# Optimization experiments

Hardware: AMD Instinct MI355X
Metric: run time of the kernel (lower is better)

## Reference

```python
import jax, jax.numpy as jnp
import numpy as np

WIDTH = 300  # CFG.width
H = 128


def _lstm_layer(x, W_ih, W_hh, b_ih, b_hh):
    # x: [B, T, D]; W_ih: [4H, D]; W_hh: [4H, H]; biases: [4H]
    B = x.shape[0]
    # precompute input contributions for all timesteps: [T, B, 4H]
    xg = jnp.einsum('btd,gd->tbg', x, W_ih) + (b_ih + b_hh)

    def step(carry, xg_t):
        h, c = carry
        g = xg_t + h @ W_hh.T  # [B, 4H]
        i, f, gg, o = jnp.split(g, 4, axis=-1)  # PyTorch gate order i,f,g,o
        i = jax.nn.sigmoid(i)
        f = jax.nn.sigmoid(f)
        gg = jnp.tanh(gg)
        o = jax.nn.sigmoid(o)
        c = f * c + i * gg
        h = o * jnp.tanh(c)
        return (h, c), h

    h0 = jnp.zeros((B, H), x.dtype)
    c0 = jnp.zeros((B, H), x.dtype)
    _, hs = jax.lax.scan(step, (h0, c0), xg)  # hs: [T, B, H]
    return jnp.transpose(hs, (1, 0, 2))  # [B, T, H]


def setup_inputs() -> dict:
    key = jax.random.key(0)
    ks = jax.random.split(key, 16)
    s = 0.05
    B, D, T = 512, 80, WIDTH
    return {
        'x': jax.random.normal(ks[0], (B, D, T), jnp.float32),
        'W_ih0': jax.random.normal(ks[1], (4 * H, D), jnp.float32) * s,
        'W_hh0': jax.random.normal(ks[2], (4 * H, H), jnp.float32) * s,
        'b_ih0': jax.random.normal(ks[3], (4 * H,), jnp.float32) * s,
        'b_hh0': jax.random.normal(ks[4], (4 * H,), jnp.float32) * s,
        'W_ih1': jax.random.normal(ks[5], (4 * H, H), jnp.float32) * s,
        'W_hh1': jax.random.normal(ks[6], (4 * H, H), jnp.float32) * s,
        'b_ih1': jax.random.normal(ks[7], (4 * H,), jnp.float32) * s,
        'b_hh1': jax.random.normal(ks[8], (4 * H,), jnp.float32) * s,
        'fc1_w': jax.random.normal(ks[9], (64, H), jnp.float32) * s,
        'fc1_b': jax.random.normal(ks[10], (64,), jnp.float32) * s,
        'fc2_w': jax.random.normal(ks[11], (32, 64), jnp.float32) * s,
        'fc2_b': jax.random.normal(ks[12], (32,), jnp.float32) * s,
        'fc3_w': jax.random.normal(ks[13], (2, 32), jnp.float32) * s,
        'fc3_b': jax.random.normal(ks[14], (2,), jnp.float32) * s,
    }


def reference(x, W_ih0, W_hh0, b_ih0, b_hh0, W_ih1, W_hh1, b_ih1, b_hh1,
              fc1_w, fc1_b, fc2_w, fc2_b, fc3_w, fc3_b):
    # input.transpose(-1,-2): [B, D, T] -> [B, T, D]
    seq = jnp.transpose(x, (0, 2, 1))
    h1 = _lstm_layer(seq, W_ih0, W_hh0, b_ih0, b_hh0)
    h2 = _lstm_layer(h1, W_ih1, W_hh1, b_ih1, b_hh1)
    out = h2[:, WIDTH - 1, :]  # [B, H]
    # _fc head (dropout is identity in eval mode)
    out = jax.nn.relu(out @ fc1_w.T + fc1_b)
    out = jax.nn.relu(out @ fc2_w.T + fc2_b)
    out = out @ fc3_w.T + fc3_b
    return out
```

## Files before the change

### kernel.cpp

```cpp
#include <hip/hip_runtime.h>


typedef _Float16 f16;
typedef _Float16 f16x8 __attribute__((ext_vector_type(8)));
typedef float f32x4 __attribute__((ext_vector_type(4)));
typedef unsigned u32x2 __attribute__((ext_vector_type(2)));

#define T_SEQ 300
#define D_IN  80
#define HDIM  128
#define B_ALL 512
#define B_TILE 16
#define N_PROD 32
#define N_WG_TOT 64

#define XT_BYTES  ((size_t)B_ALL * T_SEQ * D_IN * 2)
#define H1_BYTES  ((size_t)T_SEQ * B_ALL * HDIM * 2)
#define FLAGS_OFF (XT_BYTES + H1_BYTES)
#define FLAGS_BYTES ((size_t)N_PROD * T_SEQ * 4)
#define HSTEP_BYTES ((uint64_t)B_ALL * HDIM * 2)

__device__ __forceinline__ float sigm(float x) {
    return __builtin_amdgcn_rcpf(1.0f + __builtin_amdgcn_exp2f(-1.44269504f * x));
}
__device__ __forceinline__ float tanh_fast(float x) {
    return 1.0f - 2.0f * __builtin_amdgcn_rcpf(1.0f + __builtin_amdgcn_exp2f(2.88539008f * x));
}

__device__ __forceinline__ void wg_barrier_lds() {
    asm volatile("s_waitcnt lgkmcnt(0)" ::: "memory");
    __builtin_amdgcn_sched_barrier(0);
    __builtin_amdgcn_s_barrier();
    __builtin_amdgcn_sched_barrier(0);
}
__device__ __forceinline__ void vm_drain() {
    asm volatile("s_waitcnt vmcnt(0)" ::: "memory");
    __builtin_amdgcn_sched_barrier(0);
}

__global__ __launch_bounds__(256) void k_prep(const float* __restrict__ x,
                                              f16* __restrict__ xT) {
    __shared__ f16 tile[D_IN][T_SEQ + 8];
    const int b = blockIdx.x;
    const int tid = threadIdx.x;
    const float* xb = x + (size_t)b * D_IN * T_SEQ;
    for (int i = tid; i < D_IN * T_SEQ; i += 256) {
        int d = i / T_SEQ;
        int t = i - d * T_SEQ;
        tile[d][t] = (f16)xb[i];
    }
    __syncthreads();
    f16* outb = xT + (size_t)b * T_SEQ * D_IN;
    for (int i = tid; i < T_SEQ * (D_IN / 8); i += 256) {
        int t  = i / (D_IN / 8);
        int dc = i - t * (D_IN / 8);
        f16x8 v;
#pragma unroll
        for (int e = 0; e < 8; ++e) v[e] = tile[dc * 8 + e][t];
        *(f16x8*)(outb + t * D_IN + dc * 8) = v;
    }
}

__device__ __forceinline__ f16x8 load_wfrag(const float* __restrict__ W,
                                            int row, int ld, int k0, int kmax) {
    f16x8 v;
#pragma unroll
    for (int e = 0; e < 8; ++e) {
        int k = k0 + e;
        v[e] = (k < kmax) ? (f16)W[row * ld + k] : (f16)0.0f;
    }
    return v;
}

__global__ __launch_bounds__(512, 2) void k_lstm(
    const f16* __restrict__ xT, f16* __restrict__ h1ws, int* __restrict__ flags,
    const float* __restrict__ Wih0, const float* __restrict__ Whh0,
    const float* __restrict__ bih0, const float* __restrict__ bhh0,
    const float* __restrict__ Wih1, const float* __restrict__ Whh1,
    const float* __restrict__ bih1, const float* __restrict__ bhh1,
    const float* __restrict__ fc1w, const float* __restrict__ fc1b,
    const float* __restrict__ fc2w, const float* __restrict__ fc2b,
    const float* __restrict__ fc3w, const float* __restrict__ fc3b,
    float* __restrict__ out)
{
    const int tid = threadIdx.x;
    const int wv  = tid >> 6;
    const int l   = tid & 63;
    const int l16 = l & 15;
    const int lg  = l >> 4;
    const int wg  = blockIdx.x;
    const int u   = wv * 16 + l16;

    __shared__ __align__(16) f16 hbuf[2][16 * HDIM];
    __shared__ float h2buf[16][HDIM];
    __shared__ float a1buf[16][64];
    __shared__ float a2buf[16][33];

    for (int i = tid; i < 16 * HDIM; i += 512) hbuf[0][i] = (f16)0.0f;

    float cst[4] = {0.f, 0.f, 0.f, 0.f};

    if (wg < N_PROD) {
        const int wgb = wg;
        f16x8 wih[4][3], whh[4][4];
        float biasv[4];
#pragma unroll
        for (int nt = 0; nt < 4; ++nt) {
            int gate = nt * 128 + u;
            biasv[nt] = bih0[gate] + bhh0[gate];
#pragma unroll
            for (int kc = 0; kc < 4; ++kc)
                whh[nt][kc] = load_wfrag(Whh0, gate, HDIM, kc * 32 + lg * 8, HDIM);
#pragma unroll
            for (int kc = 0; kc < 3; ++kc)
                wih[nt][kc] = load_wfrag(Wih0, gate, D_IN, kc * 32 + lg * 8, D_IN);
        }

        const f16* xrowp = xT + (size_t)(wgb * B_TILE + l16) * T_SEQ * D_IN + lg * 8;
        const uint64_t xrowu = (uint64_t)(uintptr_t)xrowp;
        const uint64_t flagu = (uint64_t)(uintptr_t)(flags + wgb * T_SEQ);
        const int sbr = tid >> 5;
        const int sob = (tid & 31) * 8;
        const int sswz = (((sob >> 4) ^ (sbr & 7)) << 4) + (sob & 8);
        const uint64_t sdst0 = (uint64_t)(uintptr_t)h1ws +
                               (uint64_t)(wgb * B_TILE + sbr) * 256 + sob;

        f16x8 p0 = *(const f16x8*)(xrowp);
        f16x8 p1 = *(const f16x8*)(xrowp + 32);
        f16x8 p2 = *(const f16x8*)(xrowp + 64);
        f16x8 xA0 = *(const f16x8*)(xrowp + D_IN);
        f16x8 xA1 = *(const f16x8*)(xrowp + D_IN + 32);
        f16x8 xA2 = *(const f16x8*)(xrowp + D_IN + 64);
        f32x4 acc_x[4];
#pragma unroll
        for (int nt = 0; nt < 4; ++nt) {
            f32x4 a = {biasv[nt], biasv[nt], biasv[nt], biasv[nt]};
            a = __builtin_amdgcn_mfma_f32_16x16x32_f16(p0, wih[nt][0], a, 0, 0, 0);
            a = __builtin_amdgcn_mfma_f32_16x16x32_f16(p1, wih[nt][1], a, 0, 0, 0);
            a = __builtin_amdgcn_mfma_f32_16x16x32_f16(p2, wih[nt][2], a, 0, 0, 0);
            acc_x[nt] = a;
        }
        __syncthreads();

        auto pstep = [&](int t, f16x8& xc0, f16x8& xc1, f16x8& xc2,
                         f16x8& xn0, f16x8& xn1, f16x8& xn2) {
            const f16* cur = hbuf[t & 1];
            f16* nxt = hbuf[(t + 1) & 1];
            f16x8 ha[4];
#pragma unroll
            for (int kc = 0; kc < 4; ++kc) {
                int chunk = kc * 4 + lg;
                ha[kc] = *(const f16x8*)(cur + l16 * HDIM + ((chunk ^ (l16 & 7)) << 3));
            }
            if (t >= 1) {
                u32x2 hval = *(const u32x2*)((const char*)cur + sbr * 256 + sswz);
                uint64_t dst = sdst0 + (uint64_t)(t - 1) * HSTEP_BYTES;
                asm volatile("global_store_dwordx2 %0, %1, off sc0 sc1"
                             :: "v"(dst), "v"(hval) : "memory");
            }
            {
                int tl = (t + 2 < T_SEQ) ? t + 2 : T_SEQ - 1;
                uint64_t xa = xrowu + (uint64_t)tl * (D_IN * 2);
                asm volatile("global_load_dwordx4 %0, %1, off"            : "=v"(xn0) : "v"(xa) : "memory");
                asm volatile("global_load_dwordx4 %0, %1, off offset:64"  : "=v"(xn1) : "v"(xa) : "memory");
                asm volatile("global_load_dwordx4 %0, %1, off offset:128" : "=v"(xn2) : "v"(xa) : "memory");
            }
            f32x4 acc[4];
#pragma unroll
            for (int nt = 0; nt < 4; ++nt) {
                f32x4 a = acc_x[nt];
                a = __builtin_amdgcn_mfma_f32_16x16x32_f16(ha[0], whh[nt][0], a, 0, 0, 0);
                a = __builtin_amdgcn_mfma_f32_16x16x32_f16(ha[1], whh[nt][1], a, 0, 0, 0);
                a = __builtin_amdgcn_mfma_f32_16x16x32_f16(ha[2], whh[nt][2], a, 0, 0, 0);
                a = __builtin_amdgcn_mfma_f32_16x16x32_f16(ha[3], whh[nt][3], a, 0, 0, 0);
                acc[nt] = a;
            }
            asm volatile("s_waitcnt vmcnt(4)" ::: "memory");
            __builtin_amdgcn_sched_barrier(0);
#pragma unroll
            for (int nt = 0; nt < 4; ++nt) {
                f32x4 a = {biasv[nt], biasv[nt], biasv[nt], biasv[nt]};
                a = __builtin_amdgcn_mfma_f32_16x16x32_f16(xc0, wih[nt][0], a, 0, 0, 0);
                a = __builtin_amdgcn_mfma_f32_16x16x32_f16(xc1, wih[nt][1], a, 0, 0, 0);
                a = __builtin_amdgcn_mfma_f32_16x16x32_f16(xc2, wih[nt][2], a, 0, 0, 0);
                acc_x[nt] = a;
            }
#pragma unroll
            for (int r = 0; r < 4; ++r) {
                float iv = sigm(acc[0][r]);
                float fv = sigm(acc[1][r]);
                float gv = tanh_fast(acc[2][r]);
                float ov = sigm(acc[3][r]);
                float cn = fv * cst[r] + iv * gv;
                cst[r] = cn;
                f16 hh = (f16)(ov * tanh_fast(cn));
                int br = lg * 4 + r;
                nxt[br * HDIM + ((((unsigned)u >> 3) ^ (br & 7)) << 3) + (u & 7)] = hh;
            }
            asm volatile("s_waitcnt vmcnt(3)" ::: "memory");
            __builtin_amdgcn_sched_barrier(0);
            wg_barrier_lds();
            if (tid == 0 && t >= 1) {
                unsigned one = 1;
                uint64_t fa = flagu + (uint64_t)(t - 1) * 4;
                asm volatile("global_store_dword %0, %1, off sc0 sc1"
                             :: "v"(fa), "v"(one) : "memory");
            }
        };

        f16x8 xB0, xB1, xB2;
        for (int t = 0; t < T_SEQ; t += 2) {
            pstep(t,     xA0, xA1, xA2, xB0, xB1, xB2);
            pstep(t + 1, xB0, xB1, xB2, xA0, xA1, xA2);
        }
        {
            const f16* cur = hbuf[T_SEQ & 1];
            u32x2 hval = *(const u32x2*)((const char*)cur + sbr * 256 + sswz);
            uint64_t dst = sdst0 + (uint64_t)(T_SEQ - 1) * HSTEP_BYTES;
            asm volatile("global_store_dwordx2 %0, %1, off sc0 sc1"
                         :: "v"(dst), "v"(hval) : "memory");
            vm_drain();
            wg_barrier_lds();
            if (tid == 0) {
                unsigned one = 1;
                uint64_t fa = flagu + (uint64_t)(T_SEQ - 1) * 4;
                asm volatile("global_store_dword %0, %1, off sc0 sc1"
                             :: "v"(fa), "v"(one) : "memory");
            }
        }
        return;
    }

    {
        const int wgb = wg - N_PROD;
        f16x8 wih[4][4], whh[4][4];
        float biasv[4];
#pragma unroll
        for (int nt = 0; nt < 4; ++nt) {
            int gate = nt * 128 + u;
            biasv[nt] = bih1[gate] + bhh1[gate];
#pragma unroll
            for (int kc = 0; kc < 4; ++kc) {
                wih[nt][kc] = load_wfrag(Wih1, gate, HDIM, kc * 32 + lg * 8, HDIM);
                whh[nt][kc] = load_wfrag(Whh1, gate, HDIM, kc * 32 + lg * 8, HDIM);
            }
        }
        __syncthreads();

        const uint64_t flagu = (uint64_t)(uintptr_t)(flags + wgb * T_SEQ);
        const uint64_t xbase = (uint64_t)(uintptr_t)h1ws +
                               (uint64_t)(wgb * B_TILE + l16) * 256 + (uint64_t)lg * 16;

        unsigned pv = 0;
#pragma unroll 1
        for (int s = 0; s < 2; ++s) {
            uint64_t fa = flagu + (uint64_t)s * 4;
            do {
                asm volatile("global_load_dword %0, %1, off sc0 sc1"
                             : "=v"(pv) : "v"(fa) : "memory");
                asm volatile("s_waitcnt vmcnt(0)" ::: "memory");
            } while (pv == 0);
        }
        f16x8 q0, q1, q2, q3, xA0, xA1, xA2, xA3;
        {
            uint64_t a0 = xbase;
            asm volatile("global_load_dwordx4 %0, %1, off sc0 sc1"            : "=v"(q0) : "v"(a0) : "memory");
            asm volatile("global_load_dwordx4 %0, %1, off offset:64 sc0 sc1"  : "=v"(q1) : "v"(a0) : "memory");
            asm volatile("global_load_dwordx4 %0, %1, off offset:128 sc0 sc1" : "=v"(q2) : "v"(a0) : "memory");
            asm volatile("global_load_dwordx4 %0, %1, off offset:192 sc0 sc1" : "=v"(q3) : "v"(a0) : "memory");
            uint64_t a1 = xbase + HSTEP_BYTES;
            asm volatile("global_load_dwordx4 %0, %1, off sc0 sc1"            : "=v"(xA0) : "v"(a1) : "memory");
            asm volatile("global_load_dwordx4 %0, %1, off offset:64 sc0 sc1"  : "=v"(xA1) : "v"(a1) : "memory");
            asm volatile("global_load_dwordx4 %0, %1, off offset:128 sc0 sc1" : "=v"(xA2) : "v"(a1) : "memory");
            asm volatile("global_load_dwordx4 %0, %1, off offset:192 sc0 sc1" : "=v"(xA3) : "v"(a1) : "memory");
            vm_drain();
        }
        f32x4 acc_x[4];
#pragma unroll
        for (int nt = 0; nt < 4; ++nt) {
            f32x4 a = {biasv[nt], biasv[nt], biasv[nt], biasv[nt]};
            a = __builtin_amdgcn_mfma_f32_16x16x32_f16(q0, wih[nt][0], a, 0, 0, 0);
            a = __builtin_amdgcn_mfma_f32_16x16x32_f16(q1, wih[nt][1], a, 0, 0, 0);
            a = __builtin_amdgcn_mfma_f32_16x16x32_f16(q2, wih[nt][2], a, 0, 0, 0);
            a = __builtin_amdgcn_mfma_f32_16x16x32_f16(q3, wih[nt][3], a, 0, 0, 0);
            acc_x[nt] = a;
        }
        {
            uint64_t pf = flagu + 2 * 4;
            asm volatile("global_load_dword %0, %1, off sc0 sc1"
                         : "=v"(pv) : "v"(pf) : "memory");
        }

        float hlast[4] = {0.f, 0.f, 0.f, 0.f};

        auto cstep = [&](int t, f16x8& c0, f16x8& c1, f16x8& c2, f16x8& c3,
                         f16x8& n0, f16x8& n1, f16x8& n2, f16x8& n3) {
            const f16* cur = hbuf[t & 1];
            f16* nxt = hbuf[(t + 1) & 1];
            vm_drain();
            if (t + 2 < T_SEQ) {
                if (pv == 0) {
                    uint64_t fa = flagu + (uint64_t)(t + 2) * 4;
                    do {
                        asm volatile("global_load_dword %0, %1, off sc0 sc1"
                                     : "=v"(pv) : "v"(fa) : "memory");
                        asm volatile("s_waitcnt vmcnt(0)" ::: "memory");
                    } while (pv == 0);
                }
                uint64_t na = xbase + (uint64_t)(t + 2) * HSTEP_BYTES;
                asm volatile("global_load_dwordx4 %0, %1, off sc0 sc1"            : "=v"(n0) : "v"(na) : "memory");
                asm volatile("global_load_dwordx4 %0, %1, off offset:64 sc0 sc1"  : "=v"(n1) : "v"(na) : "memory");
                asm volatile("global_load_dwordx4 %0, %1, off offset:128 sc0 sc1" : "=v"(n2) : "v"(na) : "memory");
                asm volatile("global_load_dwordx4 %0, %1, off offset:192 sc0 sc1" : "=v"(n3) : "v"(na) : "memory");
                if (t + 3 < T_SEQ) {
                    uint64_t pf = flagu + (uint64_t)(t + 3) * 4;
                    asm volatile("global_load_dword %0, %1, off sc0 sc1"
                                 : "=v"(pv) : "v"(pf) : "memory");
                }
            }
            f16x8 ha[4];
#pragma unroll
            for (int kc = 0; kc < 4; ++kc) {
                int chunk = kc * 4 + lg;
                ha[kc] = *(const f16x8*)(cur + l16 * HDIM + ((chunk ^ (l16 & 7)) << 3));
            }
            f32x4 acc[4];
#pragma unroll
            for (int nt = 0; nt < 4; ++nt) {
                f32x4 a = acc_x[nt];
                a = __builtin_amdgcn_mfma_f32_16x16x32_f16(ha[0], whh[nt][0], a, 0, 0, 0);
                a = __builtin_amdgcn_mfma_f32_16x16x32_f16(ha[1], whh[nt][1], a, 0, 0, 0);
                a = __builtin_amdgcn_mfma_f32_16x16x32_f16(ha[2], whh[nt][2], a, 0, 0, 0);
                a = __builtin_amdgcn_mfma_f32_16x16x32_f16(ha[3], whh[nt][3], a, 0, 0, 0);
                acc[nt] = a;
            }
            if (t + 1 < T_SEQ) {
#pragma unroll
                for (int nt = 0; nt < 4; ++nt) {
                    f32x4 a = {biasv[nt], biasv[nt], biasv[nt], biasv[nt]};
                    a = __builtin_amdgcn_mfma_f32_16x16x32_f16(c0, wih[nt][0], a, 0, 0, 0);
                    a = __builtin_amdgcn_mfma_f32_16x16x32_f16(c1, wih[nt][1], a, 0, 0, 0);
                    a = __builtin_amdgcn_mfma_f32_16x16x32_f16(c2, wih[nt][2], a, 0, 0, 0);
                    a = __builtin_amdgcn_mfma_f32_16x16x32_f16(c3, wih[nt][3], a, 0, 0, 0);
                    acc_x[nt] = a;
                }
            }
#pragma unroll
            for (int r = 0; r < 4; ++r) {
                float iv = sigm(acc[0][r]);
                float fv = sigm(acc[1][r]);
                float gv = tanh_fast(acc[2][r]);
                float ov = sigm(acc[3][r]);
                float cn = fv * cst[r] + iv * gv;
                cst[r] = cn;
                float hv = ov * tanh_fast(cn);
                hlast[r] = hv;
                int br = lg * 4 + r;
                nxt[br * HDIM + ((((unsigned)u >> 3) ^ (br & 7)) << 3) + (u & 7)] = (f16)hv;
            }
            wg_barrier_lds();
        };

        f16x8 xB0, xB1, xB2, xB3;
        for (int t = 0; t < T_SEQ; t += 2) {
            cstep(t,     xA0, xA1, xA2, xA3, xB0, xB1, xB2, xB3);
            cstep(t + 1, xB0, xB1, xB2, xB3, xA0, xA1, xA2, xA3);
        }

#pragma unroll
        for (int r = 0; r < 4; ++r) h2buf[lg * 4 + r][u] = hlast[r];
        __syncthreads();

        for (int i = tid; i < 16 * 64; i += 512) {
            int b = i >> 6, o = i & 63;
            float s = fc1b[o];
            for (int k = 0; k < HDIM; ++k) s += h2buf[b][k] * fc1w[o * HDIM + k];
            a1buf[b][o] = fmaxf(s, 0.f);
        }
        __syncthreads();
        if (tid < 16 * 32) {
            int b = tid >> 5, o = tid & 31;
            float s = fc2b[o];
            for (int k = 0; k < 64; ++k) s += a1buf[b][k] * fc2w[o * 64 + k];
            a2buf[b][o] = fmaxf(s, 0.f);
        }
        __syncthreads();
        if (tid < 32) {
            int b = tid >> 1, o = tid & 1;
            float s = fc3b[o];
            for (int k = 0; k < 32; ++k) s += a2buf[b][k] * fc3w[o * 32 + k];
            out[(wgb * B_TILE + b) * 2 + o] = s;
        }
    }
}

extern "C" void kernel_launch(void* const* d_in, const int* in_sizes, int n_in,
                              void* d_out, int out_size, void* d_ws, size_t ws_size,
                              hipStream_t stream)
{
    const float* x    = (const float*)d_in[0];
    const float* Wih0 = (const float*)d_in[1];
    const float* Whh0 = (const float*)d_in[2];
    const float* bih0 = (const float*)d_in[3];
    const float* bhh0 = (const float*)d_in[4];
    const float* Wih1 = (const float*)d_in[5];
    const float* Whh1 = (const float*)d_in[6];
    const float* bih1 = (const float*)d_in[7];
    const float* bhh1 = (const float*)d_in[8];
    const float* fc1w = (const float*)d_in[9];
    const float* fc1b = (const float*)d_in[10];
    const float* fc2w = (const float*)d_in[11];
    const float* fc2b = (const float*)d_in[12];
    const float* fc3w = (const float*)d_in[13];
    const float* fc3b = (const float*)d_in[14];

    f16* xT    = (f16*)d_ws;
    f16* h1    = (f16*)((char*)d_ws + XT_BYTES);
    int* flags = (int*)((char*)d_ws + FLAGS_OFF);

    hipMemsetAsync(flags, 0, FLAGS_BYTES, stream);
    k_prep<<<B_ALL, 256, 0, stream>>>(x, xT);
    k_lstm<<<N_WG_TOT, 512, 0, stream>>>(xT, h1, flags, Wih0, Whh0, bih0, bhh0,
                                         Wih1, Whh1, bih1, bhh1,
                                         fc1w, fc1b, fc2w, fc2b, fc3w, fc3b,
                                         (float*)d_out);
}
```

Measured before the change: 383.0 us.

## Fuse LSTM gate math, double-buffer input projections, store h directly from registers

Replaces separate sigmoid/tanh calls with a fused gate routine that shares reciprocals, cutting transcendental and rcp ops per cell. Producer and consumer loops now ping-pong two input-projection accumulators and issue the next step's x-projection MFMAs before the recurrent MFMAs, taking them off the serial dependency chain. The producer writes h directly from registers with short stores each step, so it no longer reads back LDS to store the previous step's h. The tradeoffs are more accumulator registers, finer-grained global stores, and changed vmcnt waits that must still order the h stores before each flag is published.

```diff
diff --git a/kernel.cpp b/kernel.cpp
--- a/kernel.cpp
+++ b/kernel.cpp
@@ -4,7 +4,6 @@
 typedef _Float16 f16;
 typedef _Float16 f16x8 __attribute__((ext_vector_type(8)));
 typedef float f32x4 __attribute__((ext_vector_type(4)));
-typedef unsigned u32x2 __attribute__((ext_vector_type(2)));
 
 #define T_SEQ 300
 #define D_IN  80
@@ -20,13 +19,6 @@
 #define FLAGS_BYTES ((size_t)N_PROD * T_SEQ * 4)
 #define HSTEP_BYTES ((uint64_t)B_ALL * HDIM * 2)
 
-__device__ __forceinline__ float sigm(float x) {
-    return __builtin_amdgcn_rcpf(1.0f + __builtin_amdgcn_exp2f(-1.44269504f * x));
-}
-__device__ __forceinline__ float tanh_fast(float x) {
-    return 1.0f - 2.0f * __builtin_amdgcn_rcpf(1.0f + __builtin_amdgcn_exp2f(2.88539008f * x));
-}
-
 __device__ __forceinline__ void wg_barrier_lds() {
     asm volatile("s_waitcnt lgkmcnt(0)" ::: "memory");
     __builtin_amdgcn_sched_barrier(0);
@@ -36,6 +28,23 @@
 __device__ __forceinline__ void vm_drain() {
     asm volatile("s_waitcnt vmcnt(0)" ::: "memory");
     __builtin_amdgcn_sched_barrier(0);
+}
+__device__ __forceinline__ void vm_wait7() {
+    asm volatile("s_waitcnt vmcnt(7)" ::: "memory");
+    __builtin_amdgcn_sched_barrier(0);
+}
+
+__device__ __forceinline__ float lstm_fuse(float ai, float af, float ag, float ao,
+                                           float& c) {
+    float Ei = __builtin_amdgcn_exp2f(-1.44269504f * ai);
+    float Ef = __builtin_amdgcn_exp2f(-1.44269504f * af);
+    float Eo = __builtin_amdgcn_exp2f(-1.44269504f * ao);
+    float Eg = __builtin_amdgcn_exp2f( 2.88539008f * ag);
+    float ig = (Eg - 1.0f) * __builtin_amdgcn_rcpf((1.0f + Ei) * (Eg + 1.0f));
+    float fs = __builtin_amdgcn_rcpf(1.0f + Ef);
+    c = fs * c + ig;
+    float Ec = __builtin_amdgcn_exp2f(2.88539008f * c);
+    return (Ec - 1.0f) * __builtin_amdgcn_rcpf((1.0f + Eo) * (Ec + 1.0f));
 }
 
 __global__ __launch_bounds__(256) void k_prep(const float* __restrict__ x,
@@ -116,34 +125,37 @@
                 wih[nt][kc] = load_wfrag(Wih0, gate, D_IN, kc * 32 + lg * 8, D_IN);
         }
 
-        const f16* xrowp = xT + (size_t)(wgb * B_TILE + l16) * T_SEQ * D_IN + lg * 8;
-        const uint64_t xrowu = (uint64_t)(uintptr_t)xrowp;
+        const uint64_t xrowu = (uint64_t)(uintptr_t)(
+            xT + (size_t)(wgb * B_TILE + l16) * T_SEQ * D_IN + lg * 8);
         const uint64_t flagu = (uint64_t)(uintptr_t)(flags + wgb * T_SEQ);
-        const int sbr = tid >> 5;
-        const int sob = (tid & 31) * 8;
-        const int sswz = (((sob >> 4) ^ (sbr & 7)) << 4) + (sob & 8);
-        const uint64_t sdst0 = (uint64_t)(uintptr_t)h1ws +
-                               (uint64_t)(wgb * B_TILE + sbr) * 256 + sob;
-
-        f16x8 p0 = *(const f16x8*)(xrowp);
-        f16x8 p1 = *(const f16x8*)(xrowp + 32);
-        f16x8 p2 = *(const f16x8*)(xrowp + 64);
-        f16x8 xA0 = *(const f16x8*)(xrowp + D_IN);
-        f16x8 xA1 = *(const f16x8*)(xrowp + D_IN + 32);
-        f16x8 xA2 = *(const f16x8*)(xrowp + D_IN + 64);
-        f32x4 acc_x[4];
+        uint64_t haddr = (uint64_t)(uintptr_t)h1ws +
+                         (uint64_t)(wgb * B_TILE + lg * 4) * 256 + (uint64_t)u * 2;
+
+        f16x8 p0, p1, p2, xA0, xA1, xA2, xB0, xB1, xB2;
+        asm volatile("global_load_dwordx4 %0, %1, off"            : "=v"(p0)  : "v"(xrowu) : "memory");
+        asm volatile("global_load_dwordx4 %0, %1, off offset:64"  : "=v"(p1)  : "v"(xrowu) : "memory");
+        asm volatile("global_load_dwordx4 %0, %1, off offset:128" : "=v"(p2)  : "v"(xrowu) : "memory");
+        {
+            uint64_t xa = xrowu + (uint64_t)(D_IN * 2);
+            asm volatile("global_load_dwordx4 %0, %1, off"            : "=v"(xA0) : "v"(xa) : "memory");
+            asm volatile("global_load_dwordx4 %0, %1, off offset:64"  : "=v"(xA1) : "v"(xa) : "memory");
+            asm volatile("global_load_dwordx4 %0, %1, off offset:128" : "=v"(xA2) : "v"(xa) : "memory");
+        }
+        vm_drain();
+        f32x4 accA[4], accB[4];
 #pragma unroll
         for (int nt = 0; nt < 4; ++nt) {
             f32x4 a = {biasv[nt], biasv[nt], biasv[nt], biasv[nt]};
             a = __builtin_amdgcn_mfma_f32_16x16x32_f16(p0, wih[nt][0], a, 0, 0, 0);
             a = __builtin_amdgcn_mfma_f32_16x16x32_f16(p1, wih[nt][1], a, 0, 0, 0);
             a = __builtin_amdgcn_mfma_f32_16x16x32_f16(p2, wih[nt][2], a, 0, 0, 0);
-            acc_x[nt] = a;
+            accA[nt] = a;
         }
         __syncthreads();
 
         auto pstep = [&](int t, f16x8& xc0, f16x8& xc1, f16x8& xc2,
-                         f16x8& xn0, f16x8& xn1, f16x8& xn2) {
+                         f16x8& xn0, f16x8& xn1, f16x8& xn2,
+                         f32x4 (&accX)[4], f32x4 (&accN)[4]) {
             const f16* cur = hbuf[t & 1];
             f16* nxt = hbuf[(t + 1) & 1];
             f16x8 ha[4];
@@ -151,12 +163,6 @@
             for (int kc = 0; kc < 4; ++kc) {
                 int chunk = kc * 4 + lg;
                 ha[kc] = *(const f16x8*)(cur + l16 * HDIM + ((chunk ^ (l16 & 7)) << 3));
-            }
-            if (t >= 1) {
-                u32x2 hval = *(const u32x2*)((const char*)cur + sbr * 256 + sswz);
-                uint64_t dst = sdst0 + (uint64_t)(t - 1) * HSTEP_BYTES;
-                asm volatile("global_store_dwordx2 %0, %1, off sc0 sc1"
-                             :: "v"(dst), "v"(hval) : "memory");
             }
             {
                 int tl = (t + 2 < T_SEQ) ? t + 2 : T_SEQ - 1;
@@ -165,40 +171,40 @@
                 asm volatile("global_load_dwordx4 %0, %1, off offset:64"  : "=v"(xn1) : "v"(xa) : "memory");
                 asm volatile("global_load_dwordx4 %0, %1, off offset:128" : "=v"(xn2) : "v"(xa) : "memory");
             }
+            vm_wait7();
+#pragma unroll
+            for (int nt = 0; nt < 4; ++nt) {
+                f32x4 a = {biasv[nt], biasv[nt], biasv[nt], biasv[nt]};
+                a = __builtin_amdgcn_mfma_f32_16x16x32_f16(xc0, wih[nt][0], a, 0, 0, 0);
+                a = __builtin_amdgcn_mfma_f32_16x16x32_f16(xc1, wih[nt][1], a, 0, 0, 0);
+                a = __builtin_amdgcn_mfma_f32_16x16x32_f16(xc2, wih[nt][2], a, 0, 0, 0);
+                accN[nt] = a;
+            }
             f32x4 acc[4];
 #pragma unroll
             for (int nt = 0; nt < 4; ++nt) {
-                f32x4 a = acc_x[nt];
+                f32x4 a = accX[nt];
                 a = __builtin_amdgcn_mfma_f32_16x16x32_f16(ha[0], whh[nt][0], a, 0, 0, 0);
                 a = __builtin_amdgcn_mfma_f32_16x16x32_f16(ha[1], whh[nt][1], a, 0, 0, 0);
                 a = __builtin_amdgcn_mfma_f32_16x16x32_f16(ha[2], whh[nt][2], a, 0, 0, 0);
                 a = __builtin_amdgcn_mfma_f32_16x16x32_f16(ha[3], whh[nt][3], a, 0, 0, 0);
                 acc[nt] = a;
             }
-            asm volatile("s_waitcnt vmcnt(4)" ::: "memory");
-            __builtin_amdgcn_sched_barrier(0);
-#pragma unroll
-            for (int nt = 0; nt < 4; ++nt) {
-                f32x4 a = {biasv[nt], biasv[nt], biasv[nt], biasv[nt]};
-                a = __builtin_amdgcn_mfma_f32_16x16x32_f16(xc0, wih[nt][0], a, 0, 0, 0);
-                a = __builtin_amdgcn_mfma_f32_16x16x32_f16(xc1, wih[nt][1], a, 0, 0, 0);
-                a = __builtin_amdgcn_mfma_f32_16x16x32_f16(xc2, wih[nt][2], a, 0, 0, 0);
-                acc_x[nt] = a;
-            }
+            unsigned hb[4];
 #pragma unroll
             for (int r = 0; r < 4; ++r) {
-                float iv = sigm(acc[0][r]);
-                float fv = sigm(acc[1][r]);
-                float gv = tanh_fast(acc[2][r]);
-                float ov = sigm(acc[3][r]);
-                float cn = fv * cst[r] + iv * gv;
-                cst[r] = cn;
-                f16 hh = (f16)(ov * tanh_fast(cn));
+                float hv = lstm_fuse(acc[0][r], acc[1][r], acc[2][r], acc[3][r], cst[r]);
+                f16 hh = (f16)hv;
+                hb[r] = (unsigned)__builtin_bit_cast(unsigned short, hh);
                 int br = lg * 4 + r;
                 nxt[br * HDIM + ((((unsigned)u >> 3) ^ (br & 7)) << 3) + (u & 7)] = hh;
             }
-            asm volatile("s_waitcnt vmcnt(3)" ::: "memory");
-            __builtin_amdgcn_sched_barrier(0);
+            asm volatile("global_store_short %0, %1, off sc0 sc1"            :: "v"(haddr), "v"(hb[0]) : "memory");
+            asm volatile("global_store_short %0, %1, off offset:256 sc0 sc1" :: "v"(haddr), "v"(hb[1]) : "memory");
+            asm volatile("global_store_short %0, %1, off offset:512 sc0 sc1" :: "v"(haddr), "v"(hb[2]) : "memory");
+            asm volatile("global_store_short %0, %1, off offset:768 sc0 sc1" :: "v"(haddr), "v"(hb[3]) : "memory");
+            haddr += HSTEP_BYTES;
+            vm_wait7();
             wg_barrier_lds();
             if (tid == 0 && t >= 1) {
                 unsigned one = 1;
@@ -208,25 +214,16 @@
             }
         };
 
-        f16x8 xB0, xB1, xB2;
         for (int t = 0; t < T_SEQ; t += 2) {
-            pstep(t,     xA0, xA1, xA2, xB0, xB1, xB2);
-            pstep(t + 1, xB0, xB1, xB2, xA0, xA1, xA2);
-        }
-        {
-            const f16* cur = hbuf[T_SEQ & 1];
-            u32x2 hval = *(const u32x2*)((const char*)cur + sbr * 256 + sswz);
-            uint64_t dst = sdst0 + (uint64_t)(T_SEQ - 1) * HSTEP_BYTES;
-            asm volatile("global_store_dwordx2 %0, %1, off sc0 sc1"
-                         :: "v"(dst), "v"(hval) : "memory");
-            vm_drain();
-            wg_barrier_lds();
-            if (tid == 0) {
-                unsigned one = 1;
-                uint64_t fa = flagu + (uint64_t)(T_SEQ - 1) * 4;
-                asm volatile("global_store_dword %0, %1, off sc0 sc1"
-                             :: "v"(fa), "v"(one) : "memory");
-            }
+            pstep(t,     xA0, xA1, xA2, xB0, xB1, xB2, accA, accB);
+            pstep(t + 1, xB0, xB1, xB2, xA0, xA1, xA2, accB, accA);
+        }
+        vm_drain();
+        if (tid == 0) {
+            unsigned one = 1;
+            uint64_t fa = flagu + (uint64_t)(T_SEQ - 1) * 4;
+            asm volatile("global_store_dword %0, %1, off sc0 sc1"
+                         :: "v"(fa), "v"(one) : "memory");
         }
         return;
     }
@@ -275,7 +272,7 @@
             asm volatile("global_load_dwordx4 %0, %1, off offset:192 sc0 sc1" : "=v"(xA3) : "v"(a1) : "memory");
             vm_drain();
         }
-        f32x4 acc_x[4];
+        f32x4 accA[4], accB[4];
 #pragma unroll
         for (int nt = 0; nt < 4; ++nt) {
             f32x4 a = {biasv[nt], biasv[nt], biasv[nt], biasv[nt]};
@@ -283,7 +280,7 @@
             a = __builtin_amdgcn_mfma_f32_16x16x32_f16(q1, wih[nt][1], a, 0, 0, 0);
             a = __builtin_amdgcn_mfma_f32_16x16x32_f16(q2, wih[nt][2], a, 0, 0, 0);
             a = __builtin_amdgcn_mfma_f32_16x16x32_f16(q3, wih[nt][3], a, 0, 0, 0);
-            acc_x[nt] = a;
+            accA[nt] = a;
         }
         {
             uint64_t pf = flagu + 2 * 4;
@@ -294,9 +291,16 @@
         float hlast[4] = {0.f, 0.f, 0.f, 0.f};
 
         auto cstep = [&](int t, f16x8& c0, f16x8& c1, f16x8& c2, f16x8& c3,
-                         f16x8& n0, f16x8& n1, f16x8& n2, f16x8& n3) {
+                         f16x8& n0, f16x8& n1, f16x8& n2, f16x8& n3,
+                         f32x4 (&accX)[4], f32x4 (&accN)[4]) {
             const f16* cur = hbuf[t & 1];
             f16* nxt = hbuf[(t + 1) & 1];
+            f16x8 ha[4];
+#pragma unroll
+            for (int kc = 0; kc < 4; ++kc) {
+                int chunk = kc * 4 + lg;
+                ha[kc] = *(const f16x8*)(cur + l16 * HDIM + ((chunk ^ (l16 & 7)) << 3));
+            }
             vm_drain();
             if (t + 2 < T_SEQ) {
                 if (pv == 0) {
@@ -318,22 +322,6 @@
                                  : "=v"(pv) : "v"(pf) : "memory");
                 }
             }
-            f16x8 ha[4];
-#pragma unroll
-            for (int kc = 0; kc < 4; ++kc) {
-                int chunk = kc * 4 + lg;
-                ha[kc] = *(const f16x8*)(cur + l16 * HDIM + ((chunk ^ (l16 & 7)) << 3));
-            }
-            f32x4 acc[4];
-#pragma unroll
-            for (int nt = 0; nt < 4; ++nt) {
-                f32x4 a = acc_x[nt];
-                a = __builtin_amdgcn_mfma_f32_16x16x32_f16(ha[0], whh[nt][0], a, 0, 0, 0);
-                a = __builtin_amdgcn_mfma_f32_16x16x32_f16(ha[1], whh[nt][1], a, 0, 0, 0);
-                a = __builtin_amdgcn_mfma_f32_16x16x32_f16(ha[2], whh[nt][2], a, 0, 0, 0);
-                a = __builtin_amdgcn_mfma_f32_16x16x32_f16(ha[3], whh[nt][3], a, 0, 0, 0);
-                acc[nt] = a;
-            }
             if (t + 1 < T_SEQ) {
 #pragma unroll
                 for (int nt = 0; nt < 4; ++nt) {
@@ -342,18 +330,22 @@
                     a = __builtin_amdgcn_mfma_f32_16x16x32_f16(c1, wih[nt][1], a, 0, 0, 0);
                     a = __builtin_amdgcn_mfma_f32_16x16x32_f16(c2, wih[nt][2], a, 0, 0, 0);
                     a = __builtin_amdgcn_mfma_f32_16x16x32_f16(c3, wih[nt][3], a, 0, 0, 0);
-                    acc_x[nt] = a;
+                    accN[nt] = a;
                 }
             }
+            f32x4 acc[4];
+#pragma unroll
+            for (int nt = 0; nt < 4; ++nt) {
+                f32x4 a = accX[nt];
+                a = __builtin_amdgcn_mfma_f32_16x16x32_f16(ha[0], whh[nt][0], a, 0, 0, 0);
+                a = __builtin_amdgcn_mfma_f32_16x16x32_f16(ha[1], whh[nt][1], a, 0, 0, 0);
+                a = __builtin_amdgcn_mfma_f32_16x16x32_f16(ha[2], whh[nt][2], a, 0, 0, 0);
+                a = __builtin_amdgcn_mfma_f32_16x16x32_f16(ha[3], whh[nt][3], a, 0, 0, 0);
+                acc[nt] = a;
+            }
 #pragma unroll
             for (int r = 0; r < 4; ++r) {
-                float iv = sigm(acc[0][r]);
-                float fv = sigm(acc[1][r]);
-                float gv = tanh_fast(acc[2][r]);
-                float ov = sigm(acc[3][r]);
-                float cn = fv * cst[r] + iv * gv;
-                cst[r] = cn;
-                float hv = ov * tanh_fast(cn);
+                float hv = lstm_fuse(acc[0][r], acc[1][r], acc[2][r], acc[3][r], cst[r]);
                 hlast[r] = hv;
                 int br = lg * 4 + r;
                 nxt[br * HDIM + ((((unsigned)u >> 3) ^ (br & 7)) << 3) + (u & 7)] = (f16)hv;
@@ -363,8 +355,8 @@
 
         f16x8 xB0, xB1, xB2, xB3;
         for (int t = 0; t < T_SEQ; t += 2) {
-            cstep(t,     xA0, xA1, xA2, xA3, xB0, xB1, xB2, xB3);
-            cstep(t + 1, xB0, xB1, xB2, xB3, xA0, xA1, xA2, xA3);
+            cstep(t,     xA0, xA1, xA2, xA3, xB0, xB1, xB2, xB3, accA, accB);
+            cstep(t + 1, xB0, xB1, xB2, xB3, xA0, xA1, xA2, xA3, accB, accA);
         }
 
 #pragma unroll
```

Result: faster. 370.5 us (-3.3%).
